# Kernel optimization log

Hardware: AMD Instinct MI355X
Metric: run time of the kernel (lower is better)

The kernel has to match this reference:

```python
import jax, jax.numpy as jnp
import numpy as np

B, S, D, H = 4, 2048, 1024, 16
DK = D // H

def setup_inputs() -> dict:
    key = jax.random.key(0)
    ks = jax.random.split(key, 5)
    scale = 1.0 / np.sqrt(D)
    return {
        "x": jax.random.normal(ks[0], (B, S, D), dtype=jnp.float32),
        "Wq": jax.random.normal(ks[1], (H, D, DK), dtype=jnp.float32) * scale,
        "Wk": jax.random.normal(ks[2], (H, D, DK), dtype=jnp.float32) * scale,
        "Wv": jax.random.normal(ks[3], (H, D, DK), dtype=jnp.float32) * scale,
        "Wo": jax.random.normal(ks[4], (D, D), dtype=jnp.float32) * scale,
    }

def reference(x, Wq, Wk, Wv, Wo):
    # x: [B,S,D]; Wq/Wk/Wv: [H,D,DK] (stacked per-head Linear weights); Wo: [D,D]
    seq = x.shape[-2]
    q = jnp.einsum('bsd,hdk->bhsk', x, Wq)
    k = jnp.einsum('bsd,hdk->bhsk', x, Wk)
    v = jnp.einsum('bsd,hdk->bhsk', x, Wv)
    dk = q.shape[-1]
    scores = jnp.einsum('bhqk,bhsk->bhqs', q, k) / jnp.sqrt(jnp.asarray(dk, x.dtype))
    # causal mask: mask out strictly-future positions (triu, diagonal=1)
    causal = jnp.tril(jnp.ones((seq, seq), dtype=bool))  # True = keep
    scores = jnp.where(causal, scores, -jnp.inf)
    probs = jax.nn.softmax(scores, axis=-1)  # attn_pdrop = 0.0 -> dropout is identity
    attn = jnp.einsum('bhqs,bhsk->bhqk', probs, v)
    # concat heads: [B,S,H*DK]
    concat = attn.transpose(0, 2, 1, 3).reshape(x.shape[0], seq, -1)
    # output_proj: nn.Linear(D, D, bias=False) -> y = concat @ Wo.T
    return jnp.einsum('bsd,ed->bse', concat, Wo)
```

## Files before the change

### kernel.cpp

```cpp
#include <hip/hip_runtime.h>
#include <hip/hip_bf16.h>

#define B_ 4
#define S_ 2048
#define D_ 1024
#define H_ 16
#define DK_ 64

typedef __attribute__((ext_vector_type(8))) short bf16x8;
typedef __attribute__((ext_vector_type(4))) float f32x4;
typedef __attribute__((ext_vector_type(4))) unsigned int u32x4;

__device__ __forceinline__ unsigned short f2bf(float f) {
    unsigned int u = __float_as_uint(f);
    u += 0x7FFFu + ((u >> 16) & 1u);
    return (unsigned short)(u >> 16);
}

__device__ __forceinline__ unsigned int cvtpk_bf16(float lo, float hi) {
    unsigned int r;
    asm("v_cvt_pk_bf16_f32 %0, %1, %2" : "=v"(r) : "v"(lo), "v"(hi));
    return r;
}

#define BAR() do { __builtin_amdgcn_s_barrier(); asm volatile("" ::: "memory"); } while (0)

__global__ void cvt_kernel(const float* __restrict__ src, unsigned short* __restrict__ dst) {
    int i = (blockIdx.x * 256 + threadIdx.x) * 8;
    float4 f0 = *(const float4*)&src[i];
    float4 f1 = *(const float4*)&src[i + 4];
    unsigned short t[8] __attribute__((aligned(16))) = {
        f2bf(f0.x), f2bf(f0.y), f2bf(f0.z), f2bf(f0.w),
        f2bf(f1.x), f2bf(f1.y), f2bf(f1.z), f2bf(f1.w)};
    *(u32x4*)&dst[i] = *(const u32x4*)t;
}

__global__ void prepack_kernel(const float* __restrict__ Wq,
                               const float* __restrict__ Wk,
                               const float* __restrict__ Wv,
                               unsigned short* __restrict__ Wt) {
    __shared__ unsigned short Ts[64 * 65];
    int h = blockIdx.x, w3 = blockIdx.y, t = blockIdx.z;
    const float* src = (w3 == 0 ? Wq : (w3 == 1 ? Wk : Wv)) + h * D_ * DK_ + t * 64 * DK_;
    unsigned short* dst = Wt + (w3 * H_ + h) * DK_ * D_ + t * 64;
    const float wscale = (w3 == 0) ? 0.18033688011112042f : 1.0f;
    int tid = threadIdx.x;
    for (int rep = 0; rep < 16; ++rep) {
        int idx = rep * 256 + tid;
        int dl = idx >> 6, k = idx & 63;
        Ts[k * 65 + dl] = f2bf(src[dl * 64 + k] * wscale);
    }
    __syncthreads();
    for (int rep = 0; rep < 16; ++rep) {
        int idx = rep * 256 + tid;
        int kl = idx >> 6, dl = idx & 63;
        dst[kl * D_ + dl] = Ts[kl * 65 + dl];
    }
}

__global__ __launch_bounds__(256) void prep_kernel(const float* __restrict__ x,
                                                   const float* __restrict__ Wq,
                                                   const float* __restrict__ Wk,
                                                   const float* __restrict__ Wv,
                                                   const float* __restrict__ Wo,
                                                   unsigned short* __restrict__ xbf,
                                                   unsigned short* __restrict__ Wt,
                                                   unsigned short* __restrict__ Wobf) {
    __shared__ unsigned short Ts[64 * 65];
    const int bid = blockIdx.x;
    const int tid = threadIdx.x;
    if (bid < 4096 + 512) {
        const bool isx = bid < 4096;
        const float* src = isx ? x : Wo;
        unsigned short* dst = isx ? xbf : Wobf;
        int i = ((isx ? bid : bid - 4096) * 256 + tid) * 8;
        float4 f0 = *(const float4*)&src[i];
        float4 f1 = *(const float4*)&src[i + 4];
        unsigned short t[8] __attribute__((aligned(16))) = {
            f2bf(f0.x), f2bf(f0.y), f2bf(f0.z), f2bf(f0.w),
            f2bf(f1.x), f2bf(f1.y), f2bf(f1.z), f2bf(f1.w)};
        *(u32x4*)&dst[i] = *(const u32x4*)t;
    } else {
        const int pid = bid - 4608;
        const int h = pid & 15, w3 = (pid >> 4) % 3, t = pid / 48;
        const float* src = (w3 == 0 ? Wq : (w3 == 1 ? Wk : Wv)) + h * D_ * DK_ + t * 64 * DK_;
        unsigned short* dst = Wt + (w3 * H_ + h) * DK_ * D_ + t * 64;
        const float wscale = (w3 == 0) ? 0.18033688011112042f : 1.0f;
        for (int rep = 0; rep < 16; ++rep) {
            int idx = rep * 256 + tid;
            int dl = idx >> 6, k = idx & 63;
            Ts[k * 65 + dl] = f2bf(src[dl * 64 + k] * wscale);
        }
        __syncthreads();
        for (int rep = 0; rep < 16; ++rep) {
            int idx = rep * 256 + tid;
            int kl = idx >> 6, dl = idx & 63;
            dst[kl * D_ + dl] = Ts[kl * 65 + dl];
        }
    }
}

__device__ __forceinline__ void gload16(const unsigned short* gp, unsigned short* lp) {
    __builtin_amdgcn_global_load_lds((const __attribute__((address_space(1))) unsigned int*)gp,
                                     (__attribute__((address_space(3))) unsigned int*)lp,
                                     16, 0, 0);
}

__device__ __forceinline__ void stage_half(const unsigned short* __restrict__ g,
                                           unsigned short* slot, int h, int wv, int lane, int ldg) {
#pragma unroll
    for (int L = 0; L < 2; ++L) {
        int rbase = h * 128 + L * 64 + wv * 8;
        int r = rbase + (lane >> 3);
        int gc = (lane & 7) ^ ((lane >> 3) & 7);
        gload16(g + r * ldg + gc * 8, slot + rbase * 64);
    }
}

__device__ __forceinline__ void stageA_half(const unsigned short* __restrict__ g,
                                            unsigned short* lds_base, int wv, int lane, int ldg) {
    int r = wv * 8 + (lane >> 3);
    int gc = (lane & 7) ^ ((lane >> 3) & 7);
    gload16(g + r * ldg + gc * 8, lds_base + (wv * 8) * 64);
}

__device__ __forceinline__ void stageB_half(const unsigned short* __restrict__ g,
                                            unsigned short* lds_base, int wv, int lane, int ldg) {
#pragma unroll
    for (int L = 0; L < 2; ++L) {
        int rbase = wv * 16 + L * 8;
        int r = rbase + (lane >> 3);
        int gc = (lane & 7) ^ ((lane >> 3) & 7);
        gload16(g + r * ldg + gc * 8, lds_base + rbase * 64);
    }
}

__device__ __forceinline__ void stage64_async(const unsigned short* __restrict__ g,
                                              unsigned short* lds_base, int wv, int lane, int ldg) {
#pragma unroll
    for (int it = 0; it < 2; ++it) {
        int rbase = wv * 16 + it * 8;
        int r = rbase + (lane >> 3);
        int gc = (lane & 7) ^ ((lane >> 3) & 7);
        gload16(g + r * ldg + gc * 8, lds_base + rbase * 64);
    }
}

template <bool QKV_OUT>
__global__ __launch_bounds__(512, 2) void gemm256_kernel(const unsigned short* __restrict__ A,
                                                         const unsigned short* __restrict__ Bt,
                                                         void* __restrict__ Out,
                                                         unsigned short* __restrict__ VtOut) {
    __shared__ __align__(16) unsigned short lds[65536];
    const int tid = threadIdx.x;
    const int wv = tid >> 6, lane = tid & 63, l15 = lane & 15, q4 = lane >> 4;
    const int wm = wv >> 2, wn = wv & 3;

    const int nwg = gridDim.x * gridDim.y;
    const int bid = blockIdx.x + blockIdx.y * gridDim.x;
    const int swz = (bid & 7) * (nwg >> 3) + (bid >> 3);
    const int bx = swz % gridDim.x, by = swz / gridDim.x;
    const int r0 = bx * 256, c0 = by * 256;

    const unsigned short* Ab = A + r0 * D_;
    const unsigned short* Bb = Bt + c0 * D_;

    f32x4 acc[8][4] = {};

    stage_half(Ab, lds, 0, wv, lane, D_);
    stage_half(Bb, lds + 32768, 0, wv, lane, D_);
    stage_half(Bb, lds + 32768, 1, wv, lane, D_);
    stage_half(Ab, lds, 1, wv, lane, D_);

    for (int j = 0; j < 16; ++j) {
        const bool nx = (j + 1 < 16);
        unsigned short* Ad = lds + (j & 1) * 16384;
        unsigned short* Bd = lds + 32768 + (j & 1) * 16384;
        unsigned short* An = lds + ((j + 1) & 1) * 16384;
        unsigned short* Bn = lds + 32768 + ((j + 1) & 1) * 16384;

        bf16x8 af[4][2], bfA[2][2], bfB[2][2];

        if (nx) {
            stage_half(Ab + (j + 1) * 64, An, 0, wv, lane, D_);
            asm volatile("s_waitcnt vmcnt(6)" ::: "memory");
        } else {
            asm volatile("s_waitcnt vmcnt(4)" ::: "memory");
        }
        BAR();
#pragma unroll
        for (int kk = 0; kk < 2; ++kk) {
            const int sw = ((kk * 4 + q4) ^ (l15 & 7)) * 8;
#pragma unroll
            for (int i = 0; i < 4; ++i)
                af[i][kk] = *(const bf16x8*)&Ad[(i * 32 + wm * 16 + l15) * 64 + sw];
#pragma unroll
            for (int jf = 0; jf < 2; ++jf)
                bfA[jf][kk] = *(const bf16x8*)&Bd[(jf * 64 + wn * 16 + l15) * 64 + sw];
        }
        __builtin_amdgcn_s_setprio(1);
#pragma unroll
        for (int kk = 0; kk < 2; ++kk)
#pragma unroll
            for (int i = 0; i < 4; ++i)
#pragma unroll
                for (int jf = 0; jf < 2; ++jf)
                    acc[i][jf] = __builtin_amdgcn_mfma_f32_16x16x32_bf16(af[i][kk], bfA[jf][kk], acc[i][jf], 0, 0, 0);
        __builtin_amdgcn_s_setprio(0);

        if (nx) {
            stage_half(Bb + (j + 1) * 64, Bn, 0, wv, lane, D_);
            asm volatile("s_waitcnt vmcnt(6)" ::: "memory");
        } else {
            asm volatile("s_waitcnt vmcnt(2)" ::: "memory");
        }
        BAR();
#pragma unroll
        for (int kk = 0; kk < 2; ++kk) {
            const int sw = ((kk * 4 + q4) ^ (l15 & 7)) * 8;
#pragma unroll
            for (int jf = 0; jf < 2; ++jf)
                bfB[jf][kk] = *(const bf16x8*)&Bd[((2 + jf) * 64 + wn * 16 + l15) * 64 + sw];
        }
        __builtin_amdgcn_s_setprio(1);
#pragma unroll
        for (int kk = 0; kk < 2; ++kk)
#pragma unroll
            for (int i = 0; i < 4; ++i)
#pragma unroll
                for (int jf = 0; jf < 2; ++jf)
                    acc[i][2 + jf] = __builtin_amdgcn_mfma_f32_16x16x32_bf16(af[i][kk], bfB[jf][kk], acc[i][2 + jf], 0, 0, 0);
        __builtin_amdgcn_s_setprio(0);

        if (nx) {
            stage_half(Bb + (j + 1) * 64, Bn, 1, wv, lane, D_);
            asm volatile("s_waitcnt vmcnt(6)" ::: "memory");
        } else {
            asm volatile("s_waitcnt vmcnt(0)" ::: "memory");
        }
        BAR();
#pragma unroll
        for (int kk = 0; kk < 2; ++kk) {
            const int sw = ((kk * 4 + q4) ^ (l15 & 7)) * 8;
#pragma unroll
            for (int i = 0; i < 4; ++i)
                af[i][kk] = *(const bf16x8*)&Ad[(128 + i * 32 + wm * 16 + l15) * 64 + sw];
        }
        __builtin_amdgcn_s_setprio(1);
#pragma unroll
        for (int kk = 0; kk < 2; ++kk)
#pragma unroll
            for (int i = 0; i < 4; ++i)
#pragma unroll
                for (int jf = 0; jf < 2; ++jf)
                    acc[4 + i][2 + jf] = __builtin_amdgcn_mfma_f32_16x16x32_bf16(af[i][kk], bfB[jf][kk], acc[4 + i][2 + jf], 0, 0, 0);
        __builtin_amdgcn_s_setprio(0);

        if (nx) stage_half(Ab + (j + 1) * 64, An, 1, wv, lane, D_);
        BAR();
        __builtin_amdgcn_s_setprio(1);
#pragma unroll
        for (int kk = 0; kk < 2; ++kk)
#pragma unroll
            for (int i = 0; i < 4; ++i)
#pragma unroll
                for (int jf = 0; jf < 2; ++jf)
                    acc[4 + i][jf] = __builtin_amdgcn_mfma_f32_16x16x32_bf16(af[i][kk], bfA[jf][kk], acc[4 + i][jf], 0, 0, 0);
        __builtin_amdgcn_s_setprio(0);
    }

    __syncthreads();

    if (QKV_OUT && c0 >= 2 * D_) {
        const int b = r0 >> 11, s0 = r0 & (S_ - 1);
#pragma unroll
        for (int mh = 0; mh < 2; ++mh)
#pragma unroll
            for (int ii = 0; ii < 4; ++ii)
#pragma unroll
                for (int jf = 0; jf < 4; ++jf)
#pragma unroll
                    for (int rr = 0; rr < 4; ++rr) {
                        int cl = jf * 64 + wn * 16 + l15;
                        int rl = mh * 128 + ii * 32 + wm * 16 + q4 * 4 + rr;
                        lds[cl * 256 + (rl ^ ((cl & 7) * 8))] = f2bf(acc[mh * 4 + ii][jf][rr]);
                    }
        __syncthreads();
#pragma unroll
        for (int rep = 0; rep < 16; ++rep) {
            int idx = rep * 512 + tid;
            int col = idx >> 5, ch = idx & 31;
            u32x4 v = *(const u32x4*)&lds[col * 256 + ((ch * 8) ^ ((col & 7) * 8))];
            int gcol = c0 + col;
            int vrow = b * 1024 + (gcol & 1023);
            *(u32x4*)&VtOut[vrow * S_ + s0 + ch * 8] = v;
        }
    } else {
#pragma unroll
        for (int mh = 0; mh < 2; ++mh)
#pragma unroll
            for (int ii = 0; ii < 4; ++ii)
#pragma unroll
                for (int jf = 0; jf < 4; ++jf)
#pragma unroll
                    for (int rr = 0; rr < 4; ++rr) {
                        int grow = r0 + mh * 128 + ii * 32 + wm * 16 + q4 * 4 + rr;
                        int gcol = c0 + jf * 64 + wn * 16 + l15;
                        if (QKV_OUT) {
                            int bb = grow >> 11, s = grow & (S_ - 1);
                            int w3 = gcol >> 10, h = (gcol >> 6) & 15, dk = gcol & 63;
                            ((unsigned short*)Out)[(((w3 * B_ + bb) * H_ + h) * S_ + s) * DK_ + dk] =
                                f2bf(acc[mh * 4 + ii][jf][rr]);
                        } else {
                            ((float*)Out)[grow * D_ + gcol] = acc[mh * 4 + ii][jf][rr];
                        }
                    }
    }
}

template <int MH, int NH>
__device__ __forceinline__ void phase_mfma(const unsigned short* Asl, const unsigned short* Bsl,
                                           int db, int wm, int wn, int l15, int q4,
                                           f32x4 (&acc)[2][2][2][2]) {
    bf16x8 af[2][2], bf[2][2];
#pragma unroll
    for (int kk = 0; kk < 2; ++kk) {
        const int sw = ((kk * 4 + q4) ^ (l15 & 7)) * 8;
#pragma unroll
        for (int m4 = 0; m4 < 2; ++m4)
            af[m4][kk] = *(const bf16x8*)&Asl[(db + MH) * 4096 + (wm * 32 + m4 * 16 + l15) * 64 + sw];
#pragma unroll
        for (int n2 = 0; n2 < 2; ++n2)
            bf[n2][kk] = *(const bf16x8*)&Bsl[(db + NH) * 8192 + (wn * 32 + n2 * 16 + l15) * 64 + sw];
    }
    __builtin_amdgcn_s_setprio(1);
#pragma unroll
    for (int kk = 0; kk < 2; ++kk)
#pragma unroll
        for (int m4 = 0; m4 < 2; ++m4)
#pragma unroll
            for (int n2 = 0; n2 < 2; ++n2)
                acc[MH][NH][m4][n2] =
                    __builtin_amdgcn_mfma_f32_16x16x32_bf16(af[m4][kk], bf[n2][kk], acc[MH][NH][m4][n2], 0, 0, 0);
    __builtin_amdgcn_s_setprio(0);
}

__global__ __launch_bounds__(512) void gemm128_kernel(const unsigned short* __restrict__ A,
                                                      const unsigned short* __restrict__ Bt,
                                                      float* __restrict__ Out) {
    __shared__ __align__(16) unsigned short lds[49152];
    unsigned short* Asl = lds;
    unsigned short* Bsl = lds + 16384;

    const int tid = threadIdx.x;
    const int wv = tid >> 6, lane = tid & 63, l15 = lane & 15, q4 = lane >> 4;
    const int wm = wv >> 2, wn = wv & 3;

    const int nwg = gridDim.x * gridDim.y;
    const int bid = blockIdx.x + blockIdx.y * gridDim.x;
    const int swz = (bid & 7) * (nwg >> 3) + (bid >> 3);
    const int bx = swz % gridDim.x, by = swz / gridDim.x;
    const int r0 = bx * 128, c0 = by * 256;

    const unsigned short* Ab = A + r0 * D_;
    const unsigned short* Bb = Bt + c0 * D_;

    f32x4 acc[2][2][2][2] = {};

    stageA_half(Ab, Asl, wv, lane, D_);
    stageB_half(Bb, Bsl, wv, lane, D_);
    stageB_half(Bb + 128 * D_, Bsl + 8192, wv, lane, D_);

    for (int j = 0; j < 16; ++j) {
        const int db = (j & 1) * 2;
        const int ndb = ((j + 1) & 1) * 2;
        const bool nx = (j + 1 < 16);

        stageA_half(Ab + 64 * D_ + j * 64, Asl + (db + 1) * 4096, wv, lane, D_);
        asm volatile("s_waitcnt vmcnt(3)" ::: "memory");
        BAR();
        phase_mfma<0, 0>(Asl, Bsl, db, wm, wn, l15, q4, acc);

        if (nx) {
            stageA_half(Ab + (j + 1) * 64, Asl + (ndb + 0) * 4096, wv, lane, D_);
            asm volatile("s_waitcnt vmcnt(2)" ::: "memory");
        } else {
            asm volatile("s_waitcnt vmcnt(1)" ::: "memory");
        }
        BAR();
        phase_mfma<0, 1>(Asl, Bsl, db, wm, wn, l15, q4, acc);

        if (nx) {
            stageB_half(Bb + (j + 1) * 64, Bsl + (ndb + 0) * 8192, wv, lane, D_);
            asm volatile("s_waitcnt vmcnt(3)" ::: "memory");
        } else {
            asm volatile("s_waitcnt vmcnt(0)" ::: "memory");
        }
        BAR();
        phase_mfma<1, 1>(Asl, Bsl, db, wm, wn, l15, q4, acc);

        if (nx) stageB_half(Bb + 128 * D_ + (j + 1) * 64, Bsl + (ndb + 1) * 8192, wv, lane, D_);
        BAR();
        phase_mfma<1, 0>(Asl, Bsl, db, wm, wn, l15, q4, acc);
    }

    __syncthreads();

#pragma unroll
    for (int mh = 0; mh < 2; ++mh)
#pragma unroll
        for (int nh = 0; nh < 2; ++nh)
#pragma unroll
            for (int m4 = 0; m4 < 2; ++m4)
#pragma unroll
                for (int n2 = 0; n2 < 2; ++n2)
#pragma unroll
                    for (int rr = 0; rr < 4; ++rr) {
                        int grow = r0 + mh * 64 + wm * 32 + m4 * 16 + q4 * 4 + rr;
                        int gcol = c0 + nh * 128 + wn * 32 + n2 * 16 + l15;
                        Out[grow * D_ + gcol] = acc[mh][nh][m4][n2][rr];
                    }
}

__device__ __forceinline__ void attn_tile(const unsigned short* __restrict__ Kt,
                                          const unsigned short* __restrict__ Vtt,
                                          int k0, bool masked, int q0,
                                          int wv, int l15, int q4,
                                          const bf16x8 (&aq)[2][2],
                                          f32x4 (&o)[2][4], float (&l_)[2]) {
    f32x4 sa[2][4] = {};
    __builtin_amdgcn_s_setprio(1);
#pragma unroll
    for (int kk = 0; kk < 2; ++kk) {
        const int sw = ((kk * 4 + q4) ^ (l15 & 7)) * 8;
#pragma unroll
        for (int ct = 0; ct < 4; ++ct) {
            bf16x8 bk = *(const bf16x8*)&Kt[(ct * 16 + l15) * 64 + sw];
            sa[0][ct] = __builtin_amdgcn_mfma_f32_16x16x32_bf16(bk, aq[0][kk], sa[0][ct], 0, 0, 0);
            sa[1][ct] = __builtin_amdgcn_mfma_f32_16x16x32_bf16(bk, aq[1][kk], sa[1][ct], 0, 0, 0);
        }
    }
    __builtin_amdgcn_s_setprio(0);

    if (!masked) {
#pragma unroll
        for (int rt = 0; rt < 2; ++rt)
#pragma unroll
            for (int ct = 0; ct < 4; ++ct)
#pragma unroll
                for (int r = 0; r < 4; ++r)
                    sa[rt][ct][r] = __builtin_amdgcn_exp2f(sa[rt][ct][r]);
    } else {
        const int kb = k0 + q4 * 4;
#pragma unroll
        for (int rt = 0; rt < 2; ++rt) {
            const int qrow = q0 + wv * 32 + rt * 16 + l15;
#pragma unroll
            for (int ct = 0; ct < 4; ++ct)
#pragma unroll
                for (int r = 0; r < 4; ++r) {
                    float e = __builtin_amdgcn_exp2f(sa[rt][ct][r]);
                    sa[rt][ct][r] = (kb + ct * 16 + r <= qrow) ? e : 0.0f;
                }
        }
    }

#pragma unroll
    for (int rt = 0; rt < 2; ++rt)
#pragma unroll
        for (int ct = 0; ct < 4; ++ct)
            l_[rt] += (sa[rt][ct][0] + sa[rt][ct][1]) + (sa[rt][ct][2] + sa[rt][ct][3]);

    bf16x8 F[2][2];
#pragma unroll
    for (int rt = 0; rt < 2; ++rt)
#pragma unroll
        for (int kk = 0; kk < 2; ++kk) {
            u32x4 w;
#pragma unroll
            for (int u = 0; u < 2; ++u) {
                unsigned int a = cvtpk_bf16(sa[rt][2 * kk][2 * u], sa[rt][2 * kk][2 * u + 1]);
                unsigned int c = cvtpk_bf16(sa[rt][2 * kk + 1][2 * u], sa[rt][2 * kk + 1][2 * u + 1]);
                asm("v_permlane32_swap_b32 %0, %1" : "+v"(a), "+v"(c));
                asm("v_permlane16_swap_b32 %0, %1" : "+v"(a), "+v"(c));
                w[u] = a;
                w[2 + u] = c;
            }
            F[rt][kk] = *(const bf16x8*)&w;
        }

    __builtin_amdgcn_s_setprio(1);
#pragma unroll
    for (int kk = 0; kk < 2; ++kk) {
        const int sw = ((kk * 4 + q4) ^ (l15 & 7)) * 8;
#pragma unroll
        for (int cd = 0; cd < 4; ++cd) {
            bf16x8 bv = *(const bf16x8*)&Vtt[(cd * 16 + l15) * 64 + sw];
            o[0][cd] = __builtin_amdgcn_mfma_f32_16x16x32_bf16(F[0][kk], bv, o[0][cd], 0, 0, 0);
            o[1][cd] = __builtin_amdgcn_mfma_f32_16x16x32_bf16(F[1][kk], bv, o[1][cd], 0, 0, 0);
        }
    }
    __builtin_amdgcn_s_setprio(0);
}

__global__ __launch_bounds__(256) void attn_kernel(const unsigned short* __restrict__ qkv,
                                                   unsigned short* __restrict__ concat) {
    static const int J[16] = {15, 13, 11, 9, 0, 2, 4, 6, 14, 12, 10, 8, 1, 3, 5, 7};
    const int bh = blockIdx.x;
    const int b = bh >> 4, h = bh & 15;
    const int j = J[blockIdx.y];
    const int q0 = j * 128;
    const int np = j + 1;

    const unsigned short* Qp = qkv + ((0 * B_ + b) * H_ + h) * S_ * DK_;
    const unsigned short* Kp = qkv + ((1 * B_ + b) * H_ + h) * S_ * DK_;
    const unsigned short* Vt = qkv + 2 * B_ * H_ * S_ * DK_ + (b * H_ + h) * DK_ * S_;

    __shared__ __align__(16) unsigned short Kb[2][2][64 * 64];
    __shared__ __align__(16) unsigned short Vb[2][2][64 * 64];

    const int tid = threadIdx.x;
    const int wv = tid >> 6, lane = tid & 63, l15 = lane & 15, q4 = lane >> 4;

    bf16x8 aq[2][2];
#pragma unroll
    for (int rt = 0; rt < 2; ++rt)
#pragma unroll
        for (int kk = 0; kk < 2; ++kk)
            aq[rt][kk] = *(const bf16x8*)&Qp[(q0 + wv * 32 + rt * 16 + l15) * DK_ + kk * 32 + q4 * 8];

    __syncthreads();

    stage64_async(Kp, Kb[0][0], wv, lane, DK_);
    stage64_async(Vt, Vb[0][0], wv, lane, S_);
    stage64_async(Kp + 64 * DK_, Kb[0][1], wv, lane, DK_);
    stage64_async(Vt + 64, Vb[0][1], wv, lane, S_);

    f32x4 o[2][4] = {};
    float l_[2] = {0.0f, 0.0f};

    for (int p = 0; p < np; ++p) {
        asm volatile("s_waitcnt vmcnt(0)" ::: "memory");
        BAR();

        if (p + 1 < np) {
            const int kn = (p + 1) * 128;
            const int ns = (p + 1) & 1;
            stage64_async(Kp + kn * DK_, Kb[ns][0], wv, lane, DK_);
            stage64_async(Vt + kn, Vb[ns][0], wv, lane, S_);
            stage64_async(Kp + (kn + 64) * DK_, Kb[ns][1], wv, lane, DK_);
            stage64_async(Vt + (kn + 64), Vb[ns][1], wv, lane, S_);
        }

        const int set = p & 1;
        const bool last = (p == np - 1);
        const int k0 = p * 128;

        attn_tile(Kb[set][0], Vb[set][0], k0, last, q0, wv, l15, q4, aq, o, l_);
        if (!last || wv >= 2)
            attn_tile(Kb[set][1], Vb[set][1], k0 + 64, last, q0, wv, l15, q4, aq, o, l_);
    }

#pragma unroll
    for (int rt = 0; rt < 2; ++rt) {
        float lr = l_[rt];
        lr += __shfl_xor(lr, 16);
        lr += __shfl_xor(lr, 32);
#pragma unroll
        for (int r = 0; r < 4; ++r) {
            float lfull = __shfl(lr, (lane & 48) | (q4 * 4 + r));
            float inv = 1.0f / fmaxf(lfull, 1.0e-37f);
            int row = q0 + wv * 32 + rt * 16 + q4 * 4 + r;
#pragma unroll
            for (int cd = 0; cd < 4; ++cd) {
                int col = h * DK_ + cd * 16 + l15;
                concat[(b * S_ + row) * D_ + col] = f2bf(o[rt][cd][r] * inv);
            }
        }
    }
}

extern "C" void kernel_launch(void* const* d_in, const int* in_sizes, int n_in,
                              void* d_out, int out_size, void* d_ws, size_t ws_size,
                              hipStream_t stream) {
    const float* x  = (const float*)d_in[0];
    const float* Wq = (const float*)d_in[1];
    const float* Wk = (const float*)d_in[2];
    const float* Wv = (const float*)d_in[3];
    const float* Wo = (const float*)d_in[4];

    unsigned short* qkv    = (unsigned short*)d_ws;
    unsigned short* Wt     = qkv + 3 * B_ * H_ * S_ * DK_;
    unsigned short* xbf    = Wt + 3 * H_ * DK_ * D_;
    unsigned short* concat = xbf;
    unsigned short* VtOut  = qkv + 2 * B_ * H_ * S_ * DK_;

    const size_t need_shorts = (size_t)3 * B_ * H_ * S_ * DK_ + 3 * H_ * DK_ * D_ + B_ * S_ * D_ + D_ * D_;
    const bool sep = ws_size >= need_shorts * sizeof(unsigned short);

    if (sep) {
        unsigned short* Wobf = xbf + B_ * S_ * D_;
        prep_kernel<<<4096 + 512 + 768, 256, 0, stream>>>(x, Wq, Wk, Wv, Wo, xbf, Wt, Wobf);
        gemm256_kernel<true><<<dim3(32, 12), 512, 0, stream>>>(xbf, Wt, qkv, VtOut);
        attn_kernel<<<dim3(64, 16), 256, 0, stream>>>(qkv, concat);
        gemm128_kernel<<<dim3(64, 4), 512, 0, stream>>>(concat, Wobf, (float*)d_out);
    } else {
        unsigned short* Wobf = Wt;
        cvt_kernel<<<B_ * S_ * D_ / 2048, 256, 0, stream>>>(x, xbf);
        prepack_kernel<<<dim3(H_, 3, 16), 256, 0, stream>>>(Wq, Wk, Wv, Wt);
        gemm256_kernel<true><<<dim3(32, 12), 512, 0, stream>>>(xbf, Wt, qkv, VtOut);
        cvt_kernel<<<D_ * D_ / 2048, 256, 0, stream>>>(Wo, Wobf);
        attn_kernel<<<dim3(64, 16), 256, 0, stream>>>(qkv, concat);
        gemm128_kernel<<<dim3(64, 4), 512, 0, stream>>>(concat, Wobf, (float*)d_out);
    }
}
```

Baseline: 244.3 us.

## Process two 128-row query blocks per attention workgroup to reuse K/V tiles

Each attention workgroup now handles 256 query rows as two 128-row halves that share every staged K/V tile. This halves the grid and the K/V global loads and LDS staging per query row. Per-half causal guards skip the MFMAs for tiles past a half's diagonal. Per-thread register use doubles (two sets of Q fragments, accumulators and row sums), launch bounds now ask for two blocks per CU, and the coarser blocks may load-balance less evenly across CUs.

After: 272.0 us. +11.4%, slower.

```diff
diff --git a/kernel.cpp b/kernel.cpp
--- a/kernel.cpp
+++ b/kernel.cpp
@@ -422,13 +422,14 @@
                     }
 }
 
-__device__ __forceinline__ void attn_tile(const unsigned short* __restrict__ Kt,
-                                          const unsigned short* __restrict__ Vtt,
-                                          int k0, bool masked, int q0,
-                                          int wv, int l15, int q4,
-                                          const bf16x8 (&aq)[2][2],
-                                          f32x4 (&o)[2][4], float (&l_)[2]) {
-    f32x4 sa[2][4] = {};
+__device__ __forceinline__ void attn_tile2(const unsigned short* __restrict__ Kt,
+                                           const unsigned short* __restrict__ Vtt,
+                                           int k0, int q0,
+                                           int wv, int l15, int q4,
+                                           const bf16x8 (&aq)[2][2][2],
+                                           f32x4 (&o)[2][2][4], float (&l_)[2][2]) {
+    f32x4 sa[2][2][4] = {};
+
     __builtin_amdgcn_s_setprio(1);
 #pragma unroll
     for (int kk = 0; kk < 2; ++kk) {
@@ -436,58 +437,67 @@
 #pragma unroll
         for (int ct = 0; ct < 4; ++ct) {
             bf16x8 bk = *(const bf16x8*)&Kt[(ct * 16 + l15) * 64 + sw];
-            sa[0][ct] = __builtin_amdgcn_mfma_f32_16x16x32_bf16(bk, aq[0][kk], sa[0][ct], 0, 0, 0);
-            sa[1][ct] = __builtin_amdgcn_mfma_f32_16x16x32_bf16(bk, aq[1][kk], sa[1][ct], 0, 0, 0);
+#pragma unroll
+            for (int hh = 0; hh < 2; ++hh)
+                if (k0 < q0 + hh * 128 + 128) {
+                    sa[hh][0][ct] = __builtin_amdgcn_mfma_f32_16x16x32_bf16(bk, aq[hh][0][kk], sa[hh][0][ct], 0, 0, 0);
+                    sa[hh][1][ct] = __builtin_amdgcn_mfma_f32_16x16x32_bf16(bk, aq[hh][1][kk], sa[hh][1][ct], 0, 0, 0);
+                }
         }
     }
     __builtin_amdgcn_s_setprio(0);
 
-    if (!masked) {
+    bf16x8 F[2][2][2];
+#pragma unroll
+    for (int hh = 0; hh < 2; ++hh) {
+        const int H = q0 + hh * 128;
+        if (k0 >= H + 128) continue;
+        if (k0 + 64 <= H) {
+#pragma unroll
+            for (int rt = 0; rt < 2; ++rt)
+#pragma unroll
+                for (int ct = 0; ct < 4; ++ct)
+#pragma unroll
+                    for (int r = 0; r < 4; ++r)
+                        sa[hh][rt][ct][r] = __builtin_amdgcn_exp2f(sa[hh][rt][ct][r]);
+        } else {
+            const int kb = k0 + q4 * 4;
+#pragma unroll
+            for (int rt = 0; rt < 2; ++rt) {
+                const int qrow = H + wv * 32 + rt * 16 + l15;
+#pragma unroll
+                for (int ct = 0; ct < 4; ++ct)
+#pragma unroll
+                    for (int r = 0; r < 4; ++r) {
+                        float e = __builtin_amdgcn_exp2f(sa[hh][rt][ct][r]);
+                        sa[hh][rt][ct][r] = (kb + ct * 16 + r <= qrow) ? e : 0.0f;
+                    }
+            }
+        }
+
 #pragma unroll
         for (int rt = 0; rt < 2; ++rt)
 #pragma unroll
             for (int ct = 0; ct < 4; ++ct)
-#pragma unroll
-                for (int r = 0; r < 4; ++r)
-                    sa[rt][ct][r] = __builtin_amdgcn_exp2f(sa[rt][ct][r]);
-    } else {
-        const int kb = k0 + q4 * 4;
-#pragma unroll
-        for (int rt = 0; rt < 2; ++rt) {
-            const int qrow = q0 + wv * 32 + rt * 16 + l15;
-#pragma unroll
-            for (int ct = 0; ct < 4; ++ct)
-#pragma unroll
-                for (int r = 0; r < 4; ++r) {
-                    float e = __builtin_amdgcn_exp2f(sa[rt][ct][r]);
-                    sa[rt][ct][r] = (kb + ct * 16 + r <= qrow) ? e : 0.0f;
+                l_[hh][rt] += (sa[hh][rt][ct][0] + sa[hh][rt][ct][1]) + (sa[hh][rt][ct][2] + sa[hh][rt][ct][3]);
+
+#pragma unroll
+        for (int rt = 0; rt < 2; ++rt)
+#pragma unroll
+            for (int kk = 0; kk < 2; ++kk) {
+                u32x4 w;
+#pragma unroll
+                for (int u = 0; u < 2; ++u) {
+                    unsigned int a = cvtpk_bf16(sa[hh][rt][2 * kk][2 * u], sa[hh][rt][2 * kk][2 * u + 1]);
+                    unsigned int c = cvtpk_bf16(sa[hh][rt][2 * kk + 1][2 * u], sa[hh][rt][2 * kk + 1][2 * u + 1]);
+                    asm("v_permlane32_swap_b32 %0, %1" : "+v"(a), "+v"(c));
+                    asm("v_permlane16_swap_b32 %0, %1" : "+v"(a), "+v"(c));
+                    w[u] = a;
+                    w[2 + u] = c;
                 }
-        }
-    }
-
-#pragma unroll
-    for (int rt = 0; rt < 2; ++rt)
-#pragma unroll
-        for (int ct = 0; ct < 4; ++ct)
-            l_[rt] += (sa[rt][ct][0] + sa[rt][ct][1]) + (sa[rt][ct][2] + sa[rt][ct][3]);
-
-    bf16x8 F[2][2];
-#pragma unroll
-    for (int rt = 0; rt < 2; ++rt)
-#pragma unroll
-        for (int kk = 0; kk < 2; ++kk) {
-            u32x4 w;
-#pragma unroll
-            for (int u = 0; u < 2; ++u) {
-                unsigned int a = cvtpk_bf16(sa[rt][2 * kk][2 * u], sa[rt][2 * kk][2 * u + 1]);
-                unsigned int c = cvtpk_bf16(sa[rt][2 * kk + 1][2 * u], sa[rt][2 * kk + 1][2 * u + 1]);
-                asm("v_permlane32_swap_b32 %0, %1" : "+v"(a), "+v"(c));
-                asm("v_permlane16_swap_b32 %0, %1" : "+v"(a), "+v"(c));
-                w[u] = a;
-                w[2 + u] = c;
+                F[hh][rt][kk] = *(const bf16x8*)&w;
             }
-            F[rt][kk] = *(const bf16x8*)&w;
-        }
+    }
 
     __builtin_amdgcn_s_setprio(1);
 #pragma unroll
@@ -496,21 +506,25 @@
 #pragma unroll
         for (int cd = 0; cd < 4; ++cd) {
             bf16x8 bv = *(const bf16x8*)&Vtt[(cd * 16 + l15) * 64 + sw];
-            o[0][cd] = __builtin_amdgcn_mfma_f32_16x16x32_bf16(F[0][kk], bv, o[0][cd], 0, 0, 0);
-            o[1][cd] = __builtin_amdgcn_mfma_f32_16x16x32_bf16(F[1][kk], bv, o[1][cd], 0, 0, 0);
+#pragma unroll
+            for (int hh = 0; hh < 2; ++hh)
+                if (k0 < q0 + hh * 128 + 128) {
+                    o[hh][0][cd] = __builtin_amdgcn_mfma_f32_16x16x32_bf16(F[hh][0][kk], bv, o[hh][0][cd], 0, 0, 0);
+                    o[hh][1][cd] = __builtin_amdgcn_mfma_f32_16x16x32_bf16(F[hh][1][kk], bv, o[hh][1][cd], 0, 0, 0);
+                }
         }
     }
     __builtin_amdgcn_s_setprio(0);
 }
 
-__global__ __launch_bounds__(256) void attn_kernel(const unsigned short* __restrict__ qkv,
-                                                   unsigned short* __restrict__ concat) {
-    static const int J[16] = {15, 13, 11, 9, 0, 2, 4, 6, 14, 12, 10, 8, 1, 3, 5, 7};
+__global__ __launch_bounds__(256, 2) void attn_kernel(const unsigned short* __restrict__ qkv,
+                                                      unsigned short* __restrict__ concat) {
+    static const int J8[8] = {7, 6, 5, 4, 0, 1, 2, 3};
     const int bh = blockIdx.x;
     const int b = bh >> 4, h = bh & 15;
-    const int j = J[blockIdx.y];
-    const int q0 = j * 128;
-    const int np = j + 1;
+    const int g = J8[blockIdx.y];
+    const int q0 = g * 256;
+    const int np = 2 * g + 2;
 
     const unsigned short* Qp = qkv + ((0 * B_ + b) * H_ + h) * S_ * DK_;
     const unsigned short* Kp = qkv + ((1 * B_ + b) * H_ + h) * S_ * DK_;
@@ -522,12 +536,15 @@
     const int tid = threadIdx.x;
     const int wv = tid >> 6, lane = tid & 63, l15 = lane & 15, q4 = lane >> 4;
 
-    bf16x8 aq[2][2];
-#pragma unroll
-    for (int rt = 0; rt < 2; ++rt)
-#pragma unroll
-        for (int kk = 0; kk < 2; ++kk)
-            aq[rt][kk] = *(const bf16x8*)&Qp[(q0 + wv * 32 + rt * 16 + l15) * DK_ + kk * 32 + q4 * 8];
+    bf16x8 aq[2][2][2];
+#pragma unroll
+    for (int hh = 0; hh < 2; ++hh)
+#pragma unroll
+        for (int rt = 0; rt < 2; ++rt)
+#pragma unroll
+            for (int kk = 0; kk < 2; ++kk)
+                aq[hh][rt][kk] =
+                    *(const bf16x8*)&Qp[(q0 + hh * 128 + wv * 32 + rt * 16 + l15) * DK_ + kk * 32 + q4 * 8];
 
     __syncthreads();
 
@@ -536,8 +553,8 @@
     stage64_async(Kp + 64 * DK_, Kb[0][1], wv, lane, DK_);
     stage64_async(Vt + 64, Vb[0][1], wv, lane, S_);
 
-    f32x4 o[2][4] = {};
-    float l_[2] = {0.0f, 0.0f};
+    f32x4 o[2][2][4] = {};
+    float l_[2][2] = {};
 
     for (int p = 0; p < np; ++p) {
         asm volatile("s_waitcnt vmcnt(0)" ::: "memory");
@@ -553,31 +570,30 @@
         }
 
         const int set = p & 1;
-        const bool last = (p == np - 1);
         const int k0 = p * 128;
-
-        attn_tile(Kb[set][0], Vb[set][0], k0, last, q0, wv, l15, q4, aq, o, l_);
-        if (!last || wv >= 2)
-            attn_tile(Kb[set][1], Vb[set][1], k0 + 64, last, q0, wv, l15, q4, aq, o, l_);
-    }
-
-#pragma unroll
-    for (int rt = 0; rt < 2; ++rt) {
-        float lr = l_[rt];
-        lr += __shfl_xor(lr, 16);
-        lr += __shfl_xor(lr, 32);
-#pragma unroll
-        for (int r = 0; r < 4; ++r) {
-            float lfull = __shfl(lr, (lane & 48) | (q4 * 4 + r));
-            float inv = 1.0f / fmaxf(lfull, 1.0e-37f);
-            int row = q0 + wv * 32 + rt * 16 + q4 * 4 + r;
-#pragma unroll
-            for (int cd = 0; cd < 4; ++cd) {
-                int col = h * DK_ + cd * 16 + l15;
-                concat[(b * S_ + row) * D_ + col] = f2bf(o[rt][cd][r] * inv);
+        attn_tile2(Kb[set][0], Vb[set][0], k0, q0, wv, l15, q4, aq, o, l_);
+        attn_tile2(Kb[set][1], Vb[set][1], k0 + 64, q0, wv, l15, q4, aq, o, l_);
+    }
+
+#pragma unroll
+    for (int hh = 0; hh < 2; ++hh)
+#pragma unroll
+        for (int rt = 0; rt < 2; ++rt) {
+            float lr = l_[hh][rt];
+            lr += __shfl_xor(lr, 16);
+            lr += __shfl_xor(lr, 32);
+#pragma unroll
+            for (int r = 0; r < 4; ++r) {
+                float lfull = __shfl(lr, (lane & 48) | (q4 * 4 + r));
+                float inv = 1.0f / fmaxf(lfull, 1.0e-37f);
+                int row = q0 + hh * 128 + wv * 32 + rt * 16 + q4 * 4 + r;
+#pragma unroll
+                for (int cd = 0; cd < 4; ++cd) {
+                    int col = h * DK_ + cd * 16 + l15;
+                    concat[(b * S_ + row) * D_ + col] = f2bf(o[hh][rt][cd][r] * inv);
+                }
             }
         }
-    }
 }
 
 extern "C" void kernel_launch(void* const* d_in, const int* in_sizes, int n_in,
@@ -602,7 +618,7 @@
         unsigned short* Wobf = xbf + B_ * S_ * D_;
         prep_kernel<<<4096 + 512 + 768, 256, 0, stream>>>(x, Wq, Wk, Wv, Wo, xbf, Wt, Wobf);
         gemm256_kernel<true><<<dim3(32, 12), 512, 0, stream>>>(xbf, Wt, qkv, VtOut);
-        attn_kernel<<<dim3(64, 16), 256, 0, stream>>>(qkv, concat);
+        attn_kernel<<<dim3(64, 8), 256, 0, stream>>>(qkv, concat);
         gemm128_kernel<<<dim3(64, 4), 512, 0, stream>>>(concat, Wobf, (float*)d_out);
     } else {
         unsigned short* Wobf = Wt;
@@ -610,7 +626,7 @@
         prepack_kernel<<<dim3(H_, 3, 16), 256, 0, stream>>>(Wq, Wk, Wv, Wt);
         gemm256_kernel<true><<<dim3(32, 12), 512, 0, stream>>>(xbf, Wt, qkv, VtOut);
         cvt_kernel<<<D_ * D_ / 2048, 256, 0, stream>>>(Wo, Wobf);
-        attn_kernel<<<dim3(64, 16), 256, 0, stream>>>(qkv, concat);
+        attn_kernel<<<dim3(64, 8), 256, 0, stream>>>(qkv, concat);
         gemm128_kernel<<<dim3(64, 4), 512, 0, stream>>>(concat, Wobf, (float*)d_out);
     }
 }
```
